# Kernel optimization log

Measured on AMD Instinct MI355X. Metric: run time of the kernel, lower is better.

The kernel has to match this reference:

```python
import jax, jax.numpy as jnp
import numpy as np

BS, V, H, W = 2, 4, 24, 24
C, K, L, NH = 256, 16, 6, 8
DH = C // NH
FF = 4 * C
EPS = 1e-5


def _ln(x, w, b):
    m = jnp.mean(x, axis=-1, keepdims=True)
    v = jnp.mean((x - m) ** 2, axis=-1, keepdims=True)
    return (x - m) * jax.lax.rsqrt(v + EPS) * w + b


def _pe(x, W1, b1, W2, b2):
    # PositionEmbeddingLearnedMLP: Linear(3,C) -> ReLU -> Linear(C,C), channels-last
    return jax.nn.relu(x @ W1.T + b1) @ W2.T + b2


def setup_inputs():
    key = jax.random.key(0)
    ks = jax.random.split(key, 8)
    s = 0.02
    return {
        "feature": jax.random.normal(ks[0], (BS * V, C, H, W), jnp.float32),
        "xyz": jax.random.uniform(ks[1], (BS * V, H, W, 3), jnp.float32),
        "pe_W1": jax.random.normal(ks[2], (C, 3), jnp.float32) * s,
        "pe_b1": jnp.zeros((C,), jnp.float32),
        "pe_W2": jax.random.normal(ks[3], (C, C), jnp.float32) * s,
        "pe_b2": jnp.zeros((C,), jnp.float32),
        "Wqkv": jax.random.normal(ks[4], (L, 3 * C, C), jnp.float32) * s,
        "bqkv": jnp.zeros((L, 3 * C), jnp.float32),
        "Wo": jax.random.normal(ks[5], (L, C, C), jnp.float32) * s,
        "bo": jnp.zeros((L, C), jnp.float32),
        "ln_attn_w": jnp.ones((L, C), jnp.float32),
        "ln_attn_b": jnp.zeros((L, C), jnp.float32),
        "W1": jax.random.normal(ks[6], (L, FF, C), jnp.float32) * s,
        "b1": jnp.zeros((L, FF), jnp.float32),
        "W2": jax.random.normal(ks[7], (L, C, FF), jnp.float32) * s,
        "b2": jnp.zeros((L, C), jnp.float32),
        "ln_ffn_w": jnp.ones((L, C), jnp.float32),
        "ln_ffn_b": jnp.zeros((L, C), jnp.float32),
        "ln_out_w": jnp.ones((L, C), jnp.float32),
        "ln_out_b": jnp.zeros((L, C), jnp.float32),
    }


def _forward(feature, xyz, pe_W1, pe_b1, pe_W2, pe_b2, Wqkv, bqkv, Wo, bo,
             ln_attn_w, ln_attn_b, W1, b1, W2, b2, ln_ffn_w, ln_ffn_b,
             ln_out_w, ln_out_b):
    N = V * H * W
    # (B*V,C,H,W) -> (BS,N,C) ; (B*V,H,W,3) -> (BS,N,3) : flatten views+pixels
    feat = feature.reshape(BS, V, C, H, W).transpose(0, 1, 3, 4, 2).reshape(BS, N, C)
    pts = xyz.reshape(BS, N, 3)
    # per-batch KNN (self included), mirroring pointops.queryandgroup
    d2 = jnp.sum((pts[:, :, None, :] - pts[:, None, :, :]) ** 2, axis=-1)  # (BS,N,N)
    _, idx = jax.lax.top_k(-d2, K)  # (BS,N,K) nearest-neighbor indices
    grouped = jax.vmap(lambda p, i: p[i])(pts, idx)  # (BS,N,K,3)
    rel = grouped - pts[:, :, None, :]  # relative coords (use_xyz=True)
    q_pe = _pe(jnp.zeros((3,), feat.dtype), pe_W1, pe_b1, pe_W2, pe_b2)  # (C,)
    k_pe = _pe(rel, pe_W1, pe_b1, pe_W2, pe_b2).reshape(BS * N, K, C)
    idx_g = (idx + (jnp.arange(BS) * N)[:, None, None]).reshape(BS * N, K)
    out = feat.reshape(BS * N, C)
    for i in range(L):
        keyf = out[idx_g]  # (BN,K,C) per-layer neighbor gather
        # CrossAttentionLayer, pre-norm
        t2 = _ln(out, ln_attn_w[i], ln_attn_b[i])
        q = (t2 + q_pe) @ Wqkv[i, :C].T + bqkv[i, :C]
        k = (keyf + k_pe) @ Wqkv[i, C:2 * C].T + bqkv[i, C:2 * C]
        v = keyf @ Wqkv[i, 2 * C:].T + bqkv[i, 2 * C:]
        qh = q.reshape(-1, NH, DH)
        kh = k.reshape(-1, K, NH, DH)
        vh = v.reshape(-1, K, NH, DH)
        att = jax.nn.softmax(jnp.einsum('bhd,bkhd->bhk', qh, kh) * (DH ** -0.5), axis=-1)
        ao = jnp.einsum('bhk,bkhd->bhd', att, vh).reshape(-1, C) @ Wo[i].T + bo[i]
        out = out + ao
        # FFNLayer, pre-norm
        t2 = _ln(out, ln_ffn_w[i], ln_ffn_b[i])
        out = out + (jax.nn.relu(t2 @ W1[i].T + b1[i]) @ W2[i].T + b2[i])
        # extra per-layer LayerNorm
        out = _ln(out, ln_out_w[i], ln_out_b[i])
    return out.reshape(BS, V, H, W, C).transpose(0, 1, 4, 2, 3).reshape(BS * V, C, H, W)


def reference(feature, xyz, pe_W1, pe_b1, pe_W2, pe_b2, Wqkv, bqkv, Wo, bo,
              ln_attn_w, ln_attn_b, W1, b1, W2, b2, ln_ffn_w, ln_ffn_b,
              ln_out_w, ln_out_b):
    return _forward(feature, xyz, pe_W1, pe_b1, pe_W2, pe_b2, Wqkv, bqkv, Wo, bo,
                    ln_attn_w, ln_attn_b, W1, b1, W2, b2, ln_ffn_w, ln_ffn_b,
                    ln_out_w, ln_out_b)
```

## Files before the change

### kernel.cpp

```cpp
#include <hip/hip_runtime.h>
#include <math.h>

#define BS_ 2
#define V_ 4
#define H_ 24
#define W_ 24
#define N_ (V_*H_*W_)
#define BN_ (BS_*N_)
#define C_ 256
#define K_ 16
#define L_ 6
#define NH_ 8
#define DH_ 32
#define FF_ 1024

typedef __attribute__((ext_vector_type(4))) float f32x4;
typedef __attribute__((ext_vector_type(8))) short bf16x8;

__device__ inline unsigned short f2bf(float x) {
    unsigned u = __float_as_uint(x);
    unsigned r = u + 0x7fffu + ((u >> 16) & 1u);
    return (unsigned short)(r >> 16);
}
__device__ inline float bf2f(unsigned short h) {
    return __uint_as_float(((unsigned)h) << 16);
}

__global__ __launch_bounds__(256) void f2bf5_kernel(const float* __restrict__ s0,
                                                    const float* __restrict__ s1,
                                                    const float* __restrict__ s2,
                                                    const float* __restrict__ s3,
                                                    const float* __restrict__ s4,
                                                    unsigned short* __restrict__ dst) {
    const int c0 = 65536, c1 = 1245184, c2 = 1638400, c3 = 3211264, c4 = 4784128;
    int i = blockIdx.x*256 + threadIdx.x;
    if (i >= c4) return;
    float v;
    if (i < c0)      v = s0[i];
    else if (i < c1) v = s1[i - c0];
    else if (i < c2) v = s2[i - c1];
    else if (i < c3) v = s3[i - c2];
    else             v = s4[i - c3];
    dst[i] = f2bf(v);
}

__global__ __launch_bounds__(256) void reshape_in_kernel(const float* __restrict__ f,
                                                         float* __restrict__ outF,
                                                         unsigned short* __restrict__ outB) {
    int bn = blockIdx.x, c = threadIdx.x;
    int b = bn / N_, rem = bn % N_;
    int v = rem / (H_*W_), hw = rem % (H_*W_);
    float x = f[(((size_t)(b*V_ + v)*C_ + c)*(H_*W_)) + hw];
    outF[(size_t)bn*C_ + c] = x;
    outB[(size_t)bn*C_ + c] = f2bf(x);
}

__global__ __launch_bounds__(256) void reshape_out_kernel(const float* __restrict__ in,
                                                          float* __restrict__ o) {
    int bn = blockIdx.x, c = threadIdx.x;
    int b = bn / N_, rem = bn % N_;
    int v = rem / (H_*W_), hw = rem % (H_*W_);
    o[(((size_t)(b*V_ + v)*C_ + c)*(H_*W_)) + hw] = in[(size_t)bn*C_ + c];
}

__global__ __launch_bounds__(256) void knn_kernel(const float* __restrict__ pts,
                                                  int* __restrict__ idx) {
    int wid = threadIdx.x >> 6, lane = threadIdx.x & 63;
    int point = blockIdx.x*4 + wid;
    int b = point / N_;
    int il = point % N_;
    __shared__ float ps[N_*3];
    for (int l = threadIdx.x; l < N_*3; l += 256) ps[l] = pts[(size_t)b*N_*3 + l];
    __syncthreads();
    float qx = ps[il*3], qy = ps[il*3+1], qz = ps[il*3+2];
    unsigned long long key[36];
    #pragma unroll
    for (int s = 0; s < 36; ++s) {
        int j = lane + 64*s;
        float dx = qx - ps[j*3], dy = qy - ps[j*3+1], dz = qz - ps[j*3+2];
        float d2 = dx*dx + dy*dy + dz*dz;
        key[s] = ((unsigned long long)__float_as_uint(d2) << 32) | (unsigned)j;
    }
    for (int it = 0; it < K_; ++it) {
        unsigned long long b0 = key[0], b1 = key[1], b2 = key[2], b3 = key[3];
        #pragma unroll
        for (int s = 4; s < 36; s += 4) {
            b0 = key[s]   < b0 ? key[s]   : b0;
            b1 = key[s+1] < b1 ? key[s+1] : b1;
            b2 = key[s+2] < b2 ? key[s+2] : b2;
            b3 = key[s+3] < b3 ? key[s+3] : b3;
        }
        unsigned long long m01 = b0 < b1 ? b0 : b1;
        unsigned long long m23 = b2 < b3 ? b2 : b3;
        unsigned long long best = m01 < m23 ? m01 : m23;
        #pragma unroll
        for (int off = 32; off; off >>= 1) {
            unsigned long long o = __shfl_xor(best, off, 64);
            if (o < best) best = o;
        }
        int wj = (int)(best & 0xffffffffu);
        if (lane == 0) idx[point*K_ + it] = b*N_ + wj;
        if ((wj & 63) == lane) {
            int sw = wj >> 6;
            #pragma unroll
            for (int s = 0; s < 36; ++s) if (s == sw) key[s] = ~0ull;
        }
    }
}

__global__ __launch_bounds__(256) void qpe_kernel(const float* __restrict__ b1,
                                                  const float* __restrict__ W2,
                                                  const float* __restrict__ b2,
                                                  float* __restrict__ qpe) {
    __shared__ float h[C_];
    int tid = threadIdx.x;
    h[tid] = fmaxf(b1[tid], 0.f);
    __syncthreads();
    float acc = 0.f;
    for (int j = 0; j < C_; ++j) acc += h[j] * W2[(size_t)tid*C_ + j];
    qpe[tid] = acc + b2[tid];
}

__global__ __launch_bounds__(256) void pe_hidden_kernel(const float* __restrict__ pts,
                                                        const int* __restrict__ idx,
                                                        const float* __restrict__ W1,
                                                        const float* __restrict__ b1,
                                                        unsigned short* __restrict__ hidden) {
    int point = blockIdx.x;
    int c = threadIdx.x;
    __shared__ float rel[K_][3];
    if (threadIdx.x < K_*3) {
        int k = threadIdx.x / 3, ax = threadIdx.x % 3;
        int j = idx[point*K_ + k];
        rel[k][ax] = pts[(size_t)j*3 + ax] - pts[(size_t)point*3 + ax];
    }
    __syncthreads();
    float w0 = W1[c*3], w1 = W1[c*3+1], w2 = W1[c*3+2], bb = b1[c];
    #pragma unroll
    for (int k = 0; k < K_; ++k) {
        float v = rel[k][0]*w0 + rel[k][1]*w1 + rel[k][2]*w2 + bb;
        hidden[((size_t)point*K_ + k)*C_ + c] = f2bf(fmaxf(v, 0.f));
    }
}

template<int ACT, bool RES, int OMODE>
__device__ __forceinline__ void gemm_body(const unsigned short* __restrict__ A, int sA,
                                          const unsigned short* __restrict__ W, int sW,
                                          const float* __restrict__ bias, int bcol0,
                                          const float* __restrict__ res,
                                          float* __restrict__ outF,
                                          unsigned short* __restrict__ outB,
                                          int sO, int on0, int m0, int K) {
    __shared__ unsigned short As[2][64][40];
    __shared__ unsigned short Ws[2][64][40];
    int tid = threadIdx.x;
    int wave = tid >> 6, lane = tid & 63;
    int wr = wave >> 1, wc = wave & 1;
    f32x4 acc[2][2];
    #pragma unroll
    for (int i = 0; i < 2; ++i)
        #pragma unroll
        for (int j = 0; j < 2; ++j) acc[i][j] = (f32x4){0.f, 0.f, 0.f, 0.f};

    int r = tid >> 2, ch = tid & 3;
    const unsigned short* pA = A + (size_t)(m0 + r)*sA + ch*8;
    const unsigned short* pW = W + (size_t)r*sW + ch*8;
    *(bf16x8*)&As[0][r][ch*8] = *(const bf16x8*)pA;
    *(bf16x8*)&Ws[0][r][ch*8] = *(const bf16x8*)pW;
    __syncthreads();
    int nk = K >> 5;
    for (int t = 0; t < nk; ++t) {
        int cur = t & 1;
        bool has_next = (t + 1 < nk);
        bf16x8 la, lw;
        if (has_next) {
            la = *(const bf16x8*)(pA + (t+1)*32);
            lw = *(const bf16x8*)(pW + (t+1)*32);
        }
        int kf = (lane >> 4) * 8;
        bf16x8 af[2], wf[2];
        #pragma unroll
        for (int i = 0; i < 2; ++i) af[i] = *(const bf16x8*)&As[cur][wr*32 + i*16 + (lane & 15)][kf];
        #pragma unroll
        for (int j = 0; j < 2; ++j) wf[j] = *(const bf16x8*)&Ws[cur][wc*32 + j*16 + (lane & 15)][kf];
        #pragma unroll
        for (int i = 0; i < 2; ++i)
            #pragma unroll
            for (int j = 0; j < 2; ++j)
                acc[i][j] = __builtin_amdgcn_mfma_f32_16x16x32_bf16(af[i], wf[j], acc[i][j], 0, 0, 0);
        if (has_next) {
            *(bf16x8*)&As[cur^1][r][ch*8] = la;
            *(bf16x8*)&Ws[cur^1][r][ch*8] = lw;
        }
        __syncthreads();
    }
    #pragma unroll
    for (int i = 0; i < 2; ++i) {
        #pragma unroll
        for (int j = 0; j < 2; ++j) {
            #pragma unroll
            for (int rg = 0; rg < 4; ++rg) {
                int m = m0 + wr*32 + i*16 + (lane >> 4)*4 + rg;
                int pl = wc*32 + j*16 + (lane & 15);
                float v = acc[i][j][rg];
                if (bias) v += bias[bcol0 + pl];
                if (ACT == 1) v = fmaxf(v, 0.f);
                if (RES) v += res[(size_t)m*sO + on0 + pl];
                if (OMODE != 2) outF[(size_t)m*sO + on0 + pl] = v;
                if (OMODE != 0) outB[(size_t)m*sO + on0 + pl] = f2bf(v);
            }
        }
    }
}

template<int ACT, bool RES, int OMODE>
__global__ __launch_bounds__(256) void gemm_k(const unsigned short* __restrict__ A,
                                              const unsigned short* __restrict__ W,
                                              const float* __restrict__ bias,
                                              const float* __restrict__ res,
                                              float* __restrict__ outF,
                                              unsigned short* __restrict__ outB,
                                              int P, int K) {
    int n0 = blockIdx.x * 64, m0 = blockIdx.y * 64;
    gemm_body<ACT,RES,OMODE>(A, K, W + (size_t)n0*K, K, bias, n0, res, outF, outB, P, n0, m0, K);
}

__global__ __launch_bounds__(256) void qkv_kernel(const unsigned short* __restrict__ t2,
                                                  const unsigned short* __restrict__ outb,
                                                  const unsigned short* __restrict__ Wqkv_l,
                                                  const float* __restrict__ bqkv_l,
                                                  unsigned short* __restrict__ b_q,
                                                  unsigned short* __restrict__ b_kv) {
    int bx = blockIdx.x;
    int n0 = bx * 64;
    int m0 = blockIdx.y * 64;
    if (bx < 4) {
        gemm_body<0,false,2>(t2, C_, Wqkv_l + (size_t)n0*C_, C_, bqkv_l, n0,
                             nullptr, nullptr, b_q, 256, n0, m0, C_);
    } else {
        gemm_body<0,false,2>(outb, C_, Wqkv_l + (size_t)n0*C_, C_, bqkv_l, n0,
                             nullptr, nullptr, b_kv, 512, n0 - 256, m0, C_);
    }
}

__global__ __launch_bounds__(256) void rk_kernel(const unsigned short* __restrict__ q,
                                                 const unsigned short* __restrict__ Wqkv_l,
                                                 unsigned short* __restrict__ r) {
    int n0 = blockIdx.x * 64, m0 = blockIdx.y * 64, h = blockIdx.z;
    __shared__ unsigned short As[64][40];
    __shared__ unsigned short Ws[64][40];
    int tid = threadIdx.x;
    int wave = tid >> 6, lane = tid & 63;
    int wr = wave >> 1, wc = wave & 1;
    *(bf16x8*)&As[tid>>2][(tid&3)*8] =
        *(const bf16x8*)&q[(size_t)(m0 + (tid>>2))*C_ + h*DH_ + (tid&3)*8];
    {
        int d = tid >> 3, cg = tid & 7;
        bf16x8 wv = *(const bf16x8*)&Wqkv_l[(size_t)(C_ + h*DH_ + d)*C_ + n0 + cg*8];
        #pragma unroll
        for (int j = 0; j < 8; ++j) Ws[cg*8 + j][d] = (unsigned short)wv[j];
    }
    __syncthreads();
    int kf = (lane >> 4) * 8;
    bf16x8 af[2], wf[2];
    #pragma unroll
    for (int i = 0; i < 2; ++i) af[i] = *(const bf16x8*)&As[wr*32 + i*16 + (lane & 15)][kf];
    #pragma unroll
    for (int j = 0; j < 2; ++j) wf[j] = *(const bf16x8*)&Ws[wc*32 + j*16 + (lane & 15)][kf];
    f32x4 acc[2][2];
    #pragma unroll
    for (int i = 0; i < 2; ++i)
        #pragma unroll
        for (int j = 0; j < 2; ++j)
            acc[i][j] = __builtin_amdgcn_mfma_f32_16x16x32_bf16(af[i], wf[j],
                          (f32x4){0.f,0.f,0.f,0.f}, 0, 0, 0);
    #pragma unroll
    for (int i = 0; i < 2; ++i)
        #pragma unroll
        for (int j = 0; j < 2; ++j)
            #pragma unroll
            for (int rg = 0; rg < 4; ++rg) {
                int m = m0 + wr*32 + i*16 + (lane >> 4)*4 + rg;
                int pl = wc*32 + j*16 + (lane & 15);
                r[(size_t)m*(NH_*C_) + h*C_ + n0 + pl] = f2bf(acc[i][j][rg]);
            }
}

__global__ __launch_bounds__(256) void attn_kernel(const unsigned short* __restrict__ q,
                                                   const unsigned short* __restrict__ kv,
                                                   const unsigned short* __restrict__ kpe,
                                                   const unsigned short* __restrict__ r,
                                                   const int* __restrict__ idx,
                                                   unsigned short* __restrict__ ao) {
    int wid = threadIdx.x >> 6, lane = threadIdx.x & 63;
    int point = blockIdx.x*4 + wid;
    __shared__ __align__(16) unsigned short vs[4][K_][264];
    __shared__ __align__(16) float atts[4][NH_][K_];
    int row = lane & 15;
    int off8 = (lane >> 4) * 8;
    int idx_l = idx[point*K_ + row];

    #pragma unroll
    for (int t = 0; t < 8; ++t) {
        int vr = 2*t + (lane >> 5);
        int j = __shfl(idx_l, vr, 64);
        int cc = (lane & 31) * 8;
        *(bf16x8*)&vs[wid][vr][cc] = *(const bf16x8*)&kv[(size_t)j*512 + 256 + cc];
    }

    f32x4 acc = {0.f, 0.f, 0.f, 0.f};
    const bf16x8 zero8 = {0,0,0,0,0,0,0,0};
    #pragma unroll
    for (int s = 0; s < 8; ++s) {
        bf16x8 a = *(const bf16x8*)&kpe[((size_t)point*K_ + row)*C_ + s*32 + off8];
        bf16x8 b = zero8;
        if (row < 8) b = *(const bf16x8*)&r[(size_t)point*NH_*C_ + row*C_ + s*32 + off8];
        acc = __builtin_amdgcn_mfma_f32_16x16x32_bf16(a, b, acc, 0, 0, 0);
    }
    #pragma unroll
    for (int s = 0; s < 8; ++s) {
        bf16x8 a = *(const bf16x8*)&kv[(size_t)idx_l*512 + s*32 + off8];
        bf16x8 b = zero8;
        if (row == 8 + s) b = *(const bf16x8*)&q[(size_t)point*C_ + s*32 + off8];
        acc = __builtin_amdgcn_mfma_f32_16x16x32_bf16(a, b, acc, 0, 0, 0);
    }

    const float scale = 0.1767766952966369f;
    float sv[4], m = -1e30f;
    #pragma unroll
    for (int rg = 0; rg < 4; ++rg) {
        float o = __shfl_xor(acc[rg], 8, 64);
        sv[rg] = (acc[rg] + o) * scale;
        m = fmaxf(m, sv[rg]);
    }
    m = fmaxf(m, __shfl_xor(m, 16, 64));
    m = fmaxf(m, __shfl_xor(m, 32, 64));
    float sum = 0.f;
    #pragma unroll
    for (int rg = 0; rg < 4; ++rg) { sv[rg] = __expf(sv[rg] - m); sum += sv[rg]; }
    sum += __shfl_xor(sum, 16, 64);
    sum += __shfl_xor(sum, 32, 64);
    float inv = 1.f / sum;
    if (row < 8) {
        f32x4 av = { sv[0]*inv, sv[1]*inv, sv[2]*inv, sv[3]*inv };
        *(f32x4*)&atts[wid][row][(lane >> 4) * 4] = av;
    }

    int h = lane >> 3;
    float att_f[16];
    #pragma unroll
    for (int u = 0; u < 4; ++u) {
        f32x4 t4 = *(const f32x4*)&atts[wid][h][u*4];
        att_f[u*4+0] = t4[0]; att_f[u*4+1] = t4[1]; att_f[u*4+2] = t4[2]; att_f[u*4+3] = t4[3];
    }
    int cbase = lane * 4;
    float o0 = 0.f, o1 = 0.f, o2 = 0.f, o3 = 0.f;
    #pragma unroll
    for (int k = 0; k < K_; ++k) {
        unsigned long long vv = *(const unsigned long long*)&vs[wid][k][cbase];
        unsigned lo = (unsigned)vv, hi = (unsigned)(vv >> 32);
        float a = att_f[k];
        o0 += a * __uint_as_float(lo << 16);
        o1 += a * __uint_as_float(lo & 0xffff0000u);
        o2 += a * __uint_as_float(hi << 16);
        o3 += a * __uint_as_float(hi & 0xffff0000u);
    }
    unsigned p0 = (unsigned)f2bf(o0) | ((unsigned)f2bf(o1) << 16);
    unsigned p1 = (unsigned)f2bf(o2) | ((unsigned)f2bf(o3) << 16);
    unsigned out2[2] = { p0, p1 };
    *(unsigned long long*)&ao[(size_t)point*C_ + cbase] = *(const unsigned long long*)out2;
}

template<int OMODE>
__global__ __launch_bounds__(256) void ln_kernel(const float* __restrict__ in,
                                                 const float* __restrict__ w,
                                                 const float* __restrict__ b,
                                                 const float* __restrict__ addvec,
                                                 float* __restrict__ outF,
                                                 unsigned short* __restrict__ outB) {
    int row = blockIdx.x, tid = threadIdx.x;
    float x = in[(size_t)row*C_ + tid];
    __shared__ float red[4];
    float v = x;
    #pragma unroll
    for (int off = 32; off; off >>= 1) v += __shfl_xor(v, off, 64);
    if ((tid & 63) == 0) red[tid >> 6] = v;
    __syncthreads();
    float mean = (red[0]+red[1]+red[2]+red[3]) * (1.f/C_);
    __syncthreads();
    float dx = x - mean;
    v = dx*dx;
    #pragma unroll
    for (int off = 32; off; off >>= 1) v += __shfl_xor(v, off, 64);
    if ((tid & 63) == 0) red[tid >> 6] = v;
    __syncthreads();
    float var = (red[0]+red[1]+red[2]+red[3]) * (1.f/C_);
    float y = dx * rsqrtf(var + 1e-5f) * w[tid] + b[tid];
    if (addvec) y += addvec[tid];
    if (OMODE != 2) outF[(size_t)row*C_ + tid] = y;
    outB[(size_t)row*C_ + tid] = f2bf(y);
}

__global__ __launch_bounds__(256) void ln2_kernel(const float* __restrict__ in,
                                                  const float* __restrict__ w1, const float* __restrict__ b1v,
                                                  const float* __restrict__ w2, const float* __restrict__ b2v,
                                                  const float* __restrict__ qpe,
                                                  float* __restrict__ outF, unsigned short* __restrict__ outB,
                                                  unsigned short* __restrict__ outT2) {
    int row = blockIdx.x, tid = threadIdx.x;
    float x = in[(size_t)row*C_ + tid];
    __shared__ float red[4];
    float v = x;
    #pragma unroll
    for (int off = 32; off; off >>= 1) v += __shfl_xor(v, off, 64);
    if ((tid & 63) == 0) red[tid >> 6] = v;
    __syncthreads();
    float mean = (red[0]+red[1]+red[2]+red[3]) * (1.f/C_);
    __syncthreads();
    float dx = x - mean;
    v = dx*dx;
    #pragma unroll
    for (int off = 32; off; off >>= 1) v += __shfl_xor(v, off, 64);
    if ((tid & 63) == 0) red[tid >> 6] = v;
    __syncthreads();
    float var = (red[0]+red[1]+red[2]+red[3]) * (1.f/C_);
    float y = dx * rsqrtf(var + 1e-5f) * w1[tid] + b1v[tid];
    outF[(size_t)row*C_ + tid] = y;
    outB[(size_t)row*C_ + tid] = f2bf(y);
    v = y;
    #pragma unroll
    for (int off = 32; off; off >>= 1) v += __shfl_xor(v, off, 64);
    __syncthreads();
    if ((tid & 63) == 0) red[tid >> 6] = v;
    __syncthreads();
    float mean2 = (red[0]+red[1]+red[2]+red[3]) * (1.f/C_);
    __syncthreads();
    float dy = y - mean2;
    v = dy*dy;
    #pragma unroll
    for (int off = 32; off; off >>= 1) v += __shfl_xor(v, off, 64);
    if ((tid & 63) == 0) red[tid >> 6] = v;
    __syncthreads();
    float var2 = (red[0]+red[1]+red[2]+red[3]) * (1.f/C_);
    float z = dy * rsqrtf(var2 + 1e-5f) * w2[tid] + b2v[tid] + qpe[tid];
    outT2[(size_t)row*C_ + tid] = f2bf(z);
}

extern "C" void kernel_launch(void* const* d_in, const int* in_sizes, int n_in,
                              void* d_out, int out_size, void* d_ws, size_t ws_size,
                              hipStream_t stream) {
    const float* feature  = (const float*)d_in[0];
    const float* xyz      = (const float*)d_in[1];
    const float* pe_W1    = (const float*)d_in[2];
    const float* pe_b1    = (const float*)d_in[3];
    const float* pe_W2    = (const float*)d_in[4];
    const float* pe_b2    = (const float*)d_in[5];
    const float* Wqkv     = (const float*)d_in[6];
    const float* bqkv     = (const float*)d_in[7];
    const float* Wo       = (const float*)d_in[8];
    const float* bo       = (const float*)d_in[9];
    const float* ln_attn_w= (const float*)d_in[10];
    const float* ln_attn_b= (const float*)d_in[11];
    const float* W1       = (const float*)d_in[12];
    const float* b1       = (const float*)d_in[13];
    const float* W2       = (const float*)d_in[14];
    const float* b2       = (const float*)d_in[15];
    const float* ln_ffn_w = (const float*)d_in[16];
    const float* ln_ffn_b = (const float*)d_in[17];
    const float* ln_out_w = (const float*)d_in[18];
    const float* ln_out_b = (const float*)d_in[19];

    float* ws = (float*)d_ws;
    float* w_out = ws;
    float* w_qpe = w_out + (size_t)BN_*C_;
    unsigned short* bptr = (unsigned short*)(w_qpe + C_ + 64);
    unsigned short* b_out = bptr;  bptr += (size_t)BN_*C_;
    unsigned short* b_t2  = bptr;  bptr += (size_t)BN_*C_;
    unsigned short* b_q   = bptr;  bptr += (size_t)BN_*C_;
    unsigned short* b_kv  = bptr;  bptr += (size_t)BN_*512;
    unsigned short* b_ao  = bptr;  bptr += (size_t)BN_*C_;
    unsigned short* b_ffh = bptr;  bptr += (size_t)BN_*FF_;
    unsigned short* w_kpe = bptr;  bptr += (size_t)BN_*K_*C_;
    unsigned short* w_r   = bptr;  bptr += (size_t)BN_*NH_*C_;
    unsigned short* b_hid = bptr;  bptr += (size_t)BN_*K_*C_;
    unsigned short* bWpe  = bptr;  bptr += (size_t)C_*C_;
    unsigned short* bWqkv = bptr;  bptr += (size_t)L_*3*C_*C_;
    unsigned short* bWo   = bptr;  bptr += (size_t)L_*C_*C_;
    unsigned short* bW1   = bptr;  bptr += (size_t)L_*FF_*C_;
    unsigned short* bW2   = bptr;  bptr += (size_t)L_*C_*FF_;
    int* w_idx = (int*)bptr;

    f2bf5_kernel<<<(4784128 + 255)/256, 256, 0, stream>>>(pe_W2, Wqkv, Wo, W1, W2, bWpe);

    reshape_in_kernel<<<BN_, 256, 0, stream>>>(feature, w_out, b_out);
    knn_kernel<<<BN_/4, 256, 0, stream>>>(xyz, w_idx);
    qpe_kernel<<<1, 256, 0, stream>>>(pe_b1, pe_W2, pe_b2, w_qpe);
    pe_hidden_kernel<<<BN_, 256, 0, stream>>>(xyz, w_idx, pe_W1, pe_b1, b_hid);
    gemm_k<0,false,2><<<dim3(C_/64, (BN_*K_)/64), 256, 0, stream>>>(
        b_hid, bWpe, pe_b2, nullptr, nullptr, w_kpe, C_, C_);

    ln_kernel<2><<<BN_, 256, 0, stream>>>(w_out, ln_attn_w, ln_attn_b, w_qpe, nullptr, b_t2);

    for (int i = 0; i < L_; ++i) {
        const unsigned short* Wqkv_l = bWqkv + (size_t)i*3*C_*C_;
        const float* bqkv_l = bqkv + (size_t)i*3*C_;

        qkv_kernel<<<dim3(12, BN_/64), 256, 0, stream>>>(b_t2, b_out, Wqkv_l, bqkv_l, b_q, b_kv);
        rk_kernel<<<dim3(4, BN_/64, NH_), 256, 0, stream>>>(b_q, Wqkv_l, w_r);
        attn_kernel<<<BN_/4, 256, 0, stream>>>(b_q, b_kv, w_kpe, w_r, w_idx, b_ao);
        gemm_k<0,true,0><<<dim3(C_/64, BN_/64), 256, 0, stream>>>(
            b_ao, bWo + (size_t)i*C_*C_, bo + i*C_, w_out, w_out, nullptr, C_, C_);

        ln_kernel<2><<<BN_, 256, 0, stream>>>(w_out, ln_ffn_w + i*C_, ln_ffn_b + i*C_, nullptr, nullptr, b_t2);
        gemm_k<1,false,2><<<dim3(FF_/64, BN_/64), 256, 0, stream>>>(
            b_t2, bW1 + (size_t)i*FF_*C_, b1 + i*FF_, nullptr, nullptr, b_ffh, FF_, C_);
        gemm_k<0,true,0><<<dim3(C_/64, BN_/64), 256, 0, stream>>>(
            b_ffh, bW2 + (size_t)i*C_*FF_, b2 + i*C_, w_out, w_out, nullptr, C_, FF_);

        if (i < L_-1) {
            ln2_kernel<<<BN_, 256, 0, stream>>>(w_out, ln_out_w + i*C_, ln_out_b + i*C_,
                                                ln_attn_w + (i+1)*C_, ln_attn_b + (i+1)*C_,
                                                w_qpe, w_out, b_out, b_t2);
        } else {
            ln_kernel<1><<<BN_, 256, 0, stream>>>(w_out, ln_out_w + i*C_, ln_out_b + i*C_, nullptr, w_out, b_out);
        }
    }

    reshape_out_kernel<<<BN_, 256, 0, stream>>>(w_out, (float*)d_out);
}
```

Measured before the change: 726.9 us.

## Fuse LayerNorms into output GEMMs, PE MLP into one kernel, and input reshape with LN

Adds a gemm_ln kernel that computes full 256-column rows (16-row tiles) so the residual add and the following LayerNorm(s) run in the epilogue. This replaces the separate Wo/W2 GEMMs plus ln/ln2 kernels. The PE hidden layer is now computed in shared memory inside the kPE GEMM, so the large hidden buffer is no longer written and read back. The input reshape is fused with the first LayerNorm. Together these cut launches and global round trips, but the fused GEMM uses narrower M tiles with a larger weight-tile footprint per block, and variance is computed as E[x^2]-mean^2.

Result: faster. 682.6 us (-6.1%).

```diff
diff --git a/kernel.cpp b/kernel.cpp
--- a/kernel.cpp
+++ b/kernel.cpp
@@ -16,6 +16,7 @@
 
 typedef __attribute__((ext_vector_type(4))) float f32x4;
 typedef __attribute__((ext_vector_type(8))) short bf16x8;
+typedef __attribute__((ext_vector_type(4))) unsigned u32x4;
 
 __device__ inline unsigned short f2bf(float x) {
     unsigned u = __float_as_uint(x);
@@ -44,15 +45,36 @@
     dst[i] = f2bf(v);
 }
 
-__global__ __launch_bounds__(256) void reshape_in_kernel(const float* __restrict__ f,
-                                                         float* __restrict__ outF,
-                                                         unsigned short* __restrict__ outB) {
+__global__ __launch_bounds__(256) void reshape_in_ln(const float* __restrict__ f,
+                                                     const float* __restrict__ lnw,
+                                                     const float* __restrict__ lnb,
+                                                     const float* __restrict__ qpe,
+                                                     float* __restrict__ w_out,
+                                                     unsigned short* __restrict__ b_out,
+                                                     unsigned short* __restrict__ b_t2) {
     int bn = blockIdx.x, c = threadIdx.x;
     int b = bn / N_, rem = bn % N_;
     int v = rem / (H_*W_), hw = rem % (H_*W_);
     float x = f[(((size_t)(b*V_ + v)*C_ + c)*(H_*W_)) + hw];
-    outF[(size_t)bn*C_ + c] = x;
-    outB[(size_t)bn*C_ + c] = f2bf(x);
+    w_out[(size_t)bn*C_ + c] = x;
+    b_out[(size_t)bn*C_ + c] = f2bf(x);
+    __shared__ float red[4];
+    float s = x;
+    #pragma unroll
+    for (int off = 32; off; off >>= 1) s += __shfl_xor(s, off, 64);
+    if ((c & 63) == 0) red[c >> 6] = s;
+    __syncthreads();
+    float mean = (red[0]+red[1]+red[2]+red[3]) * (1.f/C_);
+    __syncthreads();
+    float dx = x - mean;
+    s = dx*dx;
+    #pragma unroll
+    for (int off = 32; off; off >>= 1) s += __shfl_xor(s, off, 64);
+    if ((c & 63) == 0) red[c >> 6] = s;
+    __syncthreads();
+    float var = (red[0]+red[1]+red[2]+red[3]) * (1.f/C_);
+    float y = dx * rsqrtf(var + 1e-5f) * lnw[c] + lnb[c] + qpe[c];
+    b_t2[(size_t)bn*C_ + c] = f2bf(y);
 }
 
 __global__ __launch_bounds__(256) void reshape_out_kernel(const float* __restrict__ in,
@@ -121,26 +143,89 @@
     qpe[tid] = acc + b2[tid];
 }
 
-__global__ __launch_bounds__(256) void pe_hidden_kernel(const float* __restrict__ pts,
-                                                        const int* __restrict__ idx,
-                                                        const float* __restrict__ W1,
-                                                        const float* __restrict__ b1,
-                                                        unsigned short* __restrict__ hidden) {
-    int point = blockIdx.x;
-    int c = threadIdx.x;
-    __shared__ float rel[K_][3];
-    if (threadIdx.x < K_*3) {
-        int k = threadIdx.x / 3, ax = threadIdx.x % 3;
-        int j = idx[point*K_ + k];
-        rel[k][ax] = pts[(size_t)j*3 + ax] - pts[(size_t)point*3 + ax];
-    }
-    __syncthreads();
-    float w0 = W1[c*3], w1 = W1[c*3+1], w2 = W1[c*3+2], bb = b1[c];
-    #pragma unroll
-    for (int k = 0; k < K_; ++k) {
-        float v = rel[k][0]*w0 + rel[k][1]*w1 + rel[k][2]*w2 + bb;
-        hidden[((size_t)point*K_ + k)*C_ + c] = f2bf(fmaxf(v, 0.f));
-    }
+__global__ __launch_bounds__(256) void kpe_kernel(const float* __restrict__ pts,
+                                                  const int* __restrict__ idx,
+                                                  const float* __restrict__ W1,
+                                                  const float* __restrict__ b1,
+                                                  const unsigned short* __restrict__ Wpe,
+                                                  const float* __restrict__ pb2,
+                                                  unsigned short* __restrict__ kpe) {
+    int tid = threadIdx.x;
+    int wave = tid >> 6, lane = tid & 63;
+    int wr = wave >> 1, wc = wave & 1;
+    int n0 = blockIdx.x * 64;
+    int m0 = blockIdx.y * 64;
+    __shared__ float relS[64][4];
+    __shared__ float w1S[256][4];
+    __shared__ unsigned short hid[64][264];
+    __shared__ unsigned short Ws[2][64][40];
+    w1S[tid][0] = W1[tid*3+0];
+    w1S[tid][1] = W1[tid*3+1];
+    w1S[tid][2] = W1[tid*3+2];
+    w1S[tid][3] = b1[tid];
+    if (tid < 64) {
+        int row = m0 + tid;
+        int p = row >> 4;
+        int j = idx[row];
+        relS[tid][0] = pts[(size_t)j*3+0] - pts[(size_t)p*3+0];
+        relS[tid][1] = pts[(size_t)j*3+1] - pts[(size_t)p*3+1];
+        relS[tid][2] = pts[(size_t)j*3+2] - pts[(size_t)p*3+2];
+    }
+    int rw = tid >> 2, ch = tid & 3;
+    const unsigned short* pW = Wpe + (size_t)(n0 + rw)*C_ + ch*8;
+    *(bf16x8*)&Ws[0][rw][ch*8] = *(const bf16x8*)pW;
+    __syncthreads();
+    {
+        int r = tid >> 2, cq = (tid & 3) * 64;
+        float r0 = relS[r][0], r1 = relS[r][1], r2 = relS[r][2];
+        #pragma unroll
+        for (int u8 = 0; u8 < 8; ++u8) {
+            unsigned short tmp[8];
+            #pragma unroll
+            for (int v = 0; v < 8; ++v) {
+                int c = cq + u8*8 + v;
+                f32x4 w4 = *(const f32x4*)&w1S[c][0];
+                float val = r0*w4[0] + r1*w4[1] + r2*w4[2] + w4[3];
+                tmp[v] = f2bf(fmaxf(val, 0.f));
+            }
+            *(bf16x8*)&hid[r][cq + u8*8] = *(bf16x8*)tmp;
+        }
+    }
+    __syncthreads();
+    f32x4 acc[2][2];
+    #pragma unroll
+    for (int i = 0; i < 2; ++i)
+        #pragma unroll
+        for (int j = 0; j < 2; ++j) acc[i][j] = (f32x4){0.f,0.f,0.f,0.f};
+    for (int t = 0; t < 8; ++t) {
+        int cur = t & 1;
+        bool nx = (t < 7);
+        bf16x8 lw;
+        if (nx) lw = *(const bf16x8*)(pW + (t+1)*32);
+        int kf = (lane >> 4) * 8;
+        bf16x8 af[2], wf[2];
+        #pragma unroll
+        for (int i = 0; i < 2; ++i) af[i] = *(const bf16x8*)&hid[wr*32 + i*16 + (lane & 15)][t*32 + kf];
+        #pragma unroll
+        for (int j = 0; j < 2; ++j) wf[j] = *(const bf16x8*)&Ws[cur][wc*32 + j*16 + (lane & 15)][kf];
+        #pragma unroll
+        for (int i = 0; i < 2; ++i)
+            #pragma unroll
+            for (int j = 0; j < 2; ++j)
+                acc[i][j] = __builtin_amdgcn_mfma_f32_16x16x32_bf16(af[i], wf[j], acc[i][j], 0, 0, 0);
+        if (nx) *(bf16x8*)&Ws[cur^1][rw][ch*8] = lw;
+        __syncthreads();
+    }
+    #pragma unroll
+    for (int i = 0; i < 2; ++i)
+        #pragma unroll
+        for (int j = 0; j < 2; ++j)
+            #pragma unroll
+            for (int rg = 0; rg < 4; ++rg) {
+                int mr = m0 + wr*32 + i*16 + (lane >> 4)*4 + rg;
+                int col = n0 + wc*32 + j*16 + (lane & 15);
+                kpe[(size_t)mr*C_ + col] = f2bf(acc[i][j][rg] + pb2[col]);
+            }
 }
 
 template<int ACT, bool RES, int OMODE>
@@ -243,6 +328,148 @@
     }
 }
 
+template<int VAR>
+__global__ __launch_bounds__(256) void gemm_ln(const unsigned short* __restrict__ A,
+                                               const unsigned short* __restrict__ W,
+                                               const float* __restrict__ bias,
+                                               const float* __restrict__ res,
+                                               const float* __restrict__ lnw1, const float* __restrict__ lnb1,
+                                               const float* __restrict__ lnw2, const float* __restrict__ lnb2,
+                                               const float* __restrict__ qpe,
+                                               float* __restrict__ outF,
+                                               unsigned short* __restrict__ outB,
+                                               unsigned short* __restrict__ outT2,
+                                               int K) {
+    __shared__ unsigned short Ws[2][256][40];
+    __shared__ unsigned short As[2][16][40];
+    int tid = threadIdx.x;
+    int wave = tid >> 6, lane = tid & 63;
+    int m0 = blockIdx.x * 16;
+    f32x4 acc[4];
+    #pragma unroll
+    for (int j = 0; j < 4; ++j) acc[j] = (f32x4){0.f,0.f,0.f,0.f};
+    int rw = tid >> 2, ch = tid & 3;
+    const unsigned short* pW = W + (size_t)rw*K + ch*8;
+    const unsigned short* pA = A + (size_t)(m0 + ((tid & 63) >> 2))*K + (tid & 3)*8;
+    #pragma unroll
+    for (int c = 0; c < 4; ++c)
+        *(bf16x8*)&Ws[0][c*64 + rw][ch*8] = *(const bf16x8*)(pW + (size_t)c*64*K);
+    if (tid < 64) *(bf16x8*)&As[0][tid >> 2][(tid & 3)*8] = *(const bf16x8*)pA;
+    __syncthreads();
+    int nk = K >> 5;
+    for (int t = 0; t < nk; ++t) {
+        int cur = t & 1;
+        bool nx = (t + 1 < nk);
+        bf16x8 lw0, lw1, lw2, lw3, la;
+        if (nx) {
+            lw0 = *(const bf16x8*)(pW + (size_t)0*64*K + (t+1)*32);
+            lw1 = *(const bf16x8*)(pW + (size_t)1*64*K + (t+1)*32);
+            lw2 = *(const bf16x8*)(pW + (size_t)2*64*K + (t+1)*32);
+            lw3 = *(const bf16x8*)(pW + (size_t)3*64*K + (t+1)*32);
+            if (tid < 64) la = *(const bf16x8*)(pA + (t+1)*32);
+        }
+        int kf = (lane >> 4) * 8;
+        bf16x8 af = *(const bf16x8*)&As[cur][lane & 15][kf];
+        #pragma unroll
+        for (int j = 0; j < 4; ++j) {
+            bf16x8 wf = *(const bf16x8*)&Ws[cur][wave*64 + j*16 + (lane & 15)][kf];
+            acc[j] = __builtin_amdgcn_mfma_f32_16x16x32_bf16(af, wf, acc[j], 0, 0, 0);
+        }
+        if (nx) {
+            *(bf16x8*)&Ws[cur^1][0*64 + rw][ch*8] = lw0;
+            *(bf16x8*)&Ws[cur^1][1*64 + rw][ch*8] = lw1;
+            *(bf16x8*)&Ws[cur^1][2*64 + rw][ch*8] = lw2;
+            *(bf16x8*)&Ws[cur^1][3*64 + rw][ch*8] = lw3;
+            if (tid < 64) *(bf16x8*)&As[cur^1][tid >> 2][(tid & 3)*8] = la;
+        }
+        __syncthreads();
+    }
+    float* S = (float*)&Ws[0][0][0];
+    #pragma unroll
+    for (int j = 0; j < 4; ++j) {
+        int col = wave*64 + j*16 + (lane & 15);
+        #pragma unroll
+        for (int rg = 0; rg < 4; ++rg) {
+            int row = (lane >> 4)*4 + rg;
+            S[row*260 + col] = acc[j][rg] + bias[col] + res[(size_t)(m0+row)*C_ + col];
+        }
+    }
+    __syncthreads();
+    int row = tid >> 4, g = tid & 15;
+    size_t m = m0 + row;
+    float x[16];
+    #pragma unroll
+    for (int u = 0; u < 4; ++u) {
+        f32x4 v4 = *(const f32x4*)&S[row*260 + g*16 + u*4];
+        x[u*4+0] = v4[0]; x[u*4+1] = v4[1]; x[u*4+2] = v4[2]; x[u*4+3] = v4[3];
+    }
+    float s1 = 0.f, s2 = 0.f;
+    #pragma unroll
+    for (int u = 0; u < 16; ++u) { s1 += x[u]; s2 += x[u]*x[u]; }
+    #pragma unroll
+    for (int off = 8; off; off >>= 1) { s1 += __shfl_xor(s1, off, 16); s2 += __shfl_xor(s2, off, 16); }
+    float mean = s1 * (1.f/C_);
+    float var  = s2 * (1.f/C_) - mean*mean;
+    float rstd = rsqrtf(var + 1e-5f);
+    float y1[16];
+    #pragma unroll
+    for (int u = 0; u < 4; ++u) {
+        f32x4 w4 = *(const f32x4*)&lnw1[g*16 + u*4];
+        f32x4 b4 = *(const f32x4*)&lnb1[g*16 + u*4];
+        #pragma unroll
+        for (int v = 0; v < 4; ++v)
+            y1[u*4+v] = (x[u*4+v] - mean)*rstd*w4[v] + b4[v];
+    }
+    if (VAR == 0) {
+        #pragma unroll
+        for (int u = 0; u < 4; ++u) {
+            f32x4 v4 = { x[u*4], x[u*4+1], x[u*4+2], x[u*4+3] };
+            *(f32x4*)&outF[m*C_ + g*16 + u*4] = v4;
+        }
+        unsigned pk[8];
+        #pragma unroll
+        for (int u = 0; u < 8; ++u) pk[u] = (unsigned)f2bf(y1[2*u]) | ((unsigned)f2bf(y1[2*u+1]) << 16);
+        *(u32x4*)&outT2[m*C_ + g*16]     = *(u32x4*)&pk[0];
+        *(u32x4*)&outT2[m*C_ + g*16 + 8] = *(u32x4*)&pk[4];
+    } else {
+        #pragma unroll
+        for (int u = 0; u < 4; ++u) {
+            f32x4 v4 = { y1[u*4], y1[u*4+1], y1[u*4+2], y1[u*4+3] };
+            *(f32x4*)&outF[m*C_ + g*16 + u*4] = v4;
+        }
+        if (VAR == 1) {
+            unsigned pk[8];
+            #pragma unroll
+            for (int u = 0; u < 8; ++u) pk[u] = (unsigned)f2bf(y1[2*u]) | ((unsigned)f2bf(y1[2*u+1]) << 16);
+            *(u32x4*)&outB[m*C_ + g*16]     = *(u32x4*)&pk[0];
+            *(u32x4*)&outB[m*C_ + g*16 + 8] = *(u32x4*)&pk[4];
+            float t1 = 0.f, t2s = 0.f;
+            #pragma unroll
+            for (int u = 0; u < 16; ++u) { t1 += y1[u]; t2s += y1[u]*y1[u]; }
+            #pragma unroll
+            for (int off = 8; off; off >>= 1) { t1 += __shfl_xor(t1, off, 16); t2s += __shfl_xor(t2s, off, 16); }
+            float mean2 = t1 * (1.f/C_);
+            float var2  = t2s * (1.f/C_) - mean2*mean2;
+            float rstd2 = rsqrtf(var2 + 1e-5f);
+            unsigned pk2[8];
+            #pragma unroll
+            for (int u = 0; u < 4; ++u) {
+                f32x4 w4 = *(const f32x4*)&lnw2[g*16 + u*4];
+                f32x4 b4 = *(const f32x4*)&lnb2[g*16 + u*4];
+                f32x4 q4 = *(const f32x4*)&qpe[g*16 + u*4];
+                float z0 = (y1[u*4+0]-mean2)*rstd2*w4[0] + b4[0] + q4[0];
+                float z1 = (y1[u*4+1]-mean2)*rstd2*w4[1] + b4[1] + q4[1];
+                float z2 = (y1[u*4+2]-mean2)*rstd2*w4[2] + b4[2] + q4[2];
+                float z3 = (y1[u*4+3]-mean2)*rstd2*w4[3] + b4[3] + q4[3];
+                pk2[u*2]   = (unsigned)f2bf(z0) | ((unsigned)f2bf(z1) << 16);
+                pk2[u*2+1] = (unsigned)f2bf(z2) | ((unsigned)f2bf(z3) << 16);
+            }
+            *(u32x4*)&outT2[m*C_ + g*16]     = *(u32x4*)&pk2[0];
+            *(u32x4*)&outT2[m*C_ + g*16 + 8] = *(u32x4*)&pk2[4];
+        }
+    }
+}
+
 __global__ __launch_bounds__(256) void rk_kernel(const unsigned short* __restrict__ q,
                                                  const unsigned short* __restrict__ Wqkv_l,
                                                  unsigned short* __restrict__ r) {
@@ -369,81 +596,6 @@
     unsigned p1 = (unsigned)f2bf(o2) | ((unsigned)f2bf(o3) << 16);
     unsigned out2[2] = { p0, p1 };
     *(unsigned long long*)&ao[(size_t)point*C_ + cbase] = *(const unsigned long long*)out2;
-}
-
-template<int OMODE>
-__global__ __launch_bounds__(256) void ln_kernel(const float* __restrict__ in,
-                                                 const float* __restrict__ w,
-                                                 const float* __restrict__ b,
-                                                 const float* __restrict__ addvec,
-                                                 float* __restrict__ outF,
-                                                 unsigned short* __restrict__ outB) {
-    int row = blockIdx.x, tid = threadIdx.x;
-    float x = in[(size_t)row*C_ + tid];
-    __shared__ float red[4];
-    float v = x;
-    #pragma unroll
-    for (int off = 32; off; off >>= 1) v += __shfl_xor(v, off, 64);
-    if ((tid & 63) == 0) red[tid >> 6] = v;
-    __syncthreads();
-    float mean = (red[0]+red[1]+red[2]+red[3]) * (1.f/C_);
-    __syncthreads();
-    float dx = x - mean;
-    v = dx*dx;
-    #pragma unroll
-    for (int off = 32; off; off >>= 1) v += __shfl_xor(v, off, 64);
-    if ((tid & 63) == 0) red[tid >> 6] = v;
-    __syncthreads();
-    float var = (red[0]+red[1]+red[2]+red[3]) * (1.f/C_);
-    float y = dx * rsqrtf(var + 1e-5f) * w[tid] + b[tid];
-    if (addvec) y += addvec[tid];
-    if (OMODE != 2) outF[(size_t)row*C_ + tid] = y;
-    outB[(size_t)row*C_ + tid] = f2bf(y);
-}
-
-__global__ __launch_bounds__(256) void ln2_kernel(const float* __restrict__ in,
-                                                  const float* __restrict__ w1, const float* __restrict__ b1v,
-                                                  const float* __restrict__ w2, const float* __restrict__ b2v,
-                                                  const float* __restrict__ qpe,
-                                                  float* __restrict__ outF, unsigned short* __restrict__ outB,
-                                                  unsigned short* __restrict__ outT2) {
-    int row = blockIdx.x, tid = threadIdx.x;
-    float x = in[(size_t)row*C_ + tid];
-    __shared__ float red[4];
-    float v = x;
-    #pragma unroll
-    for (int off = 32; off; off >>= 1) v += __shfl_xor(v, off, 64);
-    if ((tid & 63) == 0) red[tid >> 6] = v;
-    __syncthreads();
-    float mean = (red[0]+red[1]+red[2]+red[3]) * (1.f/C_);
-    __syncthreads();
-    float dx = x - mean;
-    v = dx*dx;
-    #pragma unroll
-    for (int off = 32; off; off >>= 1) v += __shfl_xor(v, off, 64);
-    if ((tid & 63) == 0) red[tid >> 6] = v;
-    __syncthreads();
-    float var = (red[0]+red[1]+red[2]+red[3]) * (1.f/C_);
-    float y = dx * rsqrtf(var + 1e-5f) * w1[tid] + b1v[tid];
-    outF[(size_t)row*C_ + tid] = y;
-    outB[(size_t)row*C_ + tid] = f2bf(y);
-    v = y;
-    #pragma unroll
-    for (int off = 32; off; off >>= 1) v += __shfl_xor(v, off, 64);
-    __syncthreads();
-    if ((tid & 63) == 0) red[tid >> 6] = v;
-    __syncthreads();
-    float mean2 = (red[0]+red[1]+red[2]+red[3]) * (1.f/C_);
-    __syncthreads();
-    float dy = y - mean2;
-    v = dy*dy;
-    #pragma unroll
-    for (int off = 32; off; off >>= 1) v += __shfl_xor(v, off, 64);
-    if ((tid & 63) == 0) red[tid >> 6] = v;
-    __syncthreads();
-    float var2 = (red[0]+red[1]+red[2]+red[3]) * (1.f/C_);
-    float z = dy * rsqrtf(var2 + 1e-5f) * w2[tid] + b2v[tid] + qpe[tid];
-    outT2[(size_t)row*C_ + tid] = f2bf(z);
 }
 
 extern "C" void kernel_launch(void* const* d_in, const int* in_sizes, int n_in,
@@ -482,7 +634,6 @@
     unsigned short* b_ffh = bptr;  bptr += (size_t)BN_*FF_;
     unsigned short* w_kpe = bptr;  bptr += (size_t)BN_*K_*C_;
     unsigned short* w_r   = bptr;  bptr += (size_t)BN_*NH_*C_;
-    unsigned short* b_hid = bptr;  bptr += (size_t)BN_*K_*C_;
     unsigned short* bWpe  = bptr;  bptr += (size_t)C_*C_;
     unsigned short* bWqkv = bptr;  bptr += (size_t)L_*3*C_*C_;
     unsigned short* bWo   = bptr;  bptr += (size_t)L_*C_*C_;
@@ -491,15 +642,12 @@
     int* w_idx = (int*)bptr;
 
     f2bf5_kernel<<<(4784128 + 255)/256, 256, 0, stream>>>(pe_W2, Wqkv, Wo, W1, W2, bWpe);
-
-    reshape_in_kernel<<<BN_, 256, 0, stream>>>(feature, w_out, b_out);
     knn_kernel<<<BN_/4, 256, 0, stream>>>(xyz, w_idx);
     qpe_kernel<<<1, 256, 0, stream>>>(pe_b1, pe_W2, pe_b2, w_qpe);
-    pe_hidden_kernel<<<BN_, 256, 0, stream>>>(xyz, w_idx, pe_W1, pe_b1, b_hid);
-    gemm_k<0,false,2><<<dim3(C_/64, (BN_*K_)/64), 256, 0, stream>>>(
-        b_hid, bWpe, pe_b2, nullptr, nullptr, w_kpe, C_, C_);
-
-    ln_kernel<2><<<BN_, 256, 0, stream>>>(w_out, ln_attn_w, ln_attn_b, w_qpe, nullptr, b_t2);
+    reshape_in_ln<<<BN_, 256, 0, stream>>>(feature, ln_attn_w, ln_attn_b, w_qpe,
+                                           w_out, b_out, b_t2);
+    kpe_kernel<<<dim3(C_/64, (BN_*K_)/64), 256, 0, stream>>>(xyz, w_idx, pe_W1, pe_b1,
+                                                             bWpe, pe_b2, w_kpe);
 
     for (int i = 0; i < L_; ++i) {
         const unsigned short* Wqkv_l = bWqkv + (size_t)i*3*C_*C_;
@@ -508,21 +656,23 @@
         qkv_kernel<<<dim3(12, BN_/64), 256, 0, stream>>>(b_t2, b_out, Wqkv_l, bqkv_l, b_q, b_kv);
         rk_kernel<<<dim3(4, BN_/64, NH_), 256, 0, stream>>>(b_q, Wqkv_l, w_r);
         attn_kernel<<<BN_/4, 256, 0, stream>>>(b_q, b_kv, w_kpe, w_r, w_idx, b_ao);
-        gemm_k<0,true,0><<<dim3(C_/64, BN_/64), 256, 0, stream>>>(
-            b_ao, bWo + (size_t)i*C_*C_, bo + i*C_, w_out, w_out, nullptr, C_, C_);
-
-        ln_kernel<2><<<BN_, 256, 0, stream>>>(w_out, ln_ffn_w + i*C_, ln_ffn_b + i*C_, nullptr, nullptr, b_t2);
+        gemm_ln<0><<<BN_/16, 256, 0, stream>>>(
+            b_ao, bWo + (size_t)i*C_*C_, bo + i*C_, w_out,
+            ln_ffn_w + i*C_, ln_ffn_b + i*C_, nullptr, nullptr, nullptr,
+            w_out, nullptr, b_t2, C_);
         gemm_k<1,false,2><<<dim3(FF_/64, BN_/64), 256, 0, stream>>>(
             b_t2, bW1 + (size_t)i*FF_*C_, b1 + i*FF_, nullptr, nullptr, b_ffh, FF_, C_);
-        gemm_k<0,true,0><<<dim3(C_/64, BN_/64), 256, 0, stream>>>(
-            b_ffh, bW2 + (size_t)i*C_*FF_, b2 + i*C_, w_out, w_out, nullptr, C_, FF_);
-
         if (i < L_-1) {
-            ln2_kernel<<<BN_, 256, 0, stream>>>(w_out, ln_out_w + i*C_, ln_out_b + i*C_,
-                                                ln_attn_w + (i+1)*C_, ln_attn_b + (i+1)*C_,
-                                                w_qpe, w_out, b_out, b_t2);
+            gemm_ln<1><<<BN_/16, 256, 0, stream>>>(
+                b_ffh, bW2 + (size_t)i*C_*FF_, b2 + i*C_, w_out,
+                ln_out_w + i*C_, ln_out_b + i*C_,
+                ln_attn_w + (i+1)*C_, ln_attn_b + (i+1)*C_, w_qpe,
+                w_out, b_out, b_t2, FF_);
         } else {
-            ln_kernel<1><<<BN_, 256, 0, stream>>>(w_out, ln_out_w + i*C_, ln_out_b + i*C_, nullptr, w_out, b_out);
+            gemm_ln<2><<<BN_/16, 256, 0, stream>>>(
+                b_ffh, bW2 + (size_t)i*C_*FF_, b2 + i*C_, w_out,
+                ln_out_w + i*C_, ln_out_b + i*C_, nullptr, nullptr, nullptr,
+                w_out, nullptr, nullptr, FF_);
         }
     }
 
```
